# Performance work log

Hardware: AMD Instinct MI355X
Metric: run time of the kernel (lower is better)

## Reference

```python
import jax, jax.numpy as jnp
import numpy as np

B, N, CIN, COUT = 2, 150000, 64, 64
SPATIAL = (128, 128, 128)  # spatial_shape forward arg, fixed here (list arg)
EPS = 1e-5


def setup_inputs() -> dict:
    key = jax.random.key(0)
    k1, k2, k3 = jax.random.split(key, 3)
    features = jax.random.normal(k1, (B, N, CIN), jnp.float32)
    coordinates = jax.random.randint(k2, (B, N, 3), 0, SPATIAL[0], jnp.int32)
    # SparseConv3d weight: 3x3x3 kernel flattened to 27 offsets, [27, Cin, Cout]
    weight = jax.random.normal(k3, (27, CIN, COUT), jnp.float32) * 0.05
    gamma = jnp.ones((COUT,), jnp.float32)
    beta = jnp.zeros((COUT,), jnp.float32)
    return {"features": features, "coordinates": coordinates, "weight": weight,
            "gamma": gamma, "beta": beta, "batch_size": B}


def _rulebook_ids(coordinates, batch_size):
    """For each of 27 kernel offsets, the flat input-point id feeding each output
    site (output sites = input sites, rulebook gather). Empty/OOB -> BN (zero row)."""
    X, Y, Z = SPATIAL
    Np = coordinates.shape[1]
    BN = batch_size * Np
    pid = jnp.arange(BN, dtype=jnp.int32)
    b = jnp.repeat(jnp.arange(batch_size, dtype=jnp.int32), Np)
    c = coordinates.reshape(-1, 3)
    # dense voxel hash: coord -> point id (max for deterministic collision handling)
    grid = jnp.full((batch_size, X, Y, Z), -1, jnp.int32)
    grid = grid.at[b, c[:, 0], c[:, 1], c[:, 2]].max(pid)
    # 27 offsets in {-1,0,1}^3 (padding=1, kernel=3, stride=1)
    r = jnp.arange(-1, 2, dtype=jnp.int32)
    offs = jnp.stack(jnp.meshgrid(r, r, r, indexing="ij"), -1).reshape(27, 3)
    nc = c[None, :, :] + offs[:, None, :]                      # [27, BN, 3]
    hi = jnp.array([X, Y, Z], jnp.int32)
    valid = jnp.all((nc >= 0) & (nc < hi), axis=-1)            # [27, BN]
    ncc = jnp.clip(nc, 0, hi - 1)
    ids = grid[b[None, :], ncc[..., 0], ncc[..., 1], ncc[..., 2]]
    return jnp.where(valid & (ids >= 0), ids, BN)              # BN -> zero row


def reference(features, coordinates, weight, gamma, beta, batch_size):
    Bs, Np, Cin = features.shape
    BN = Bs * Np
    ids = _rulebook_ids(coordinates, batch_size)               # [27, BN]
    feats = jnp.concatenate(
        [features.reshape(BN, Cin), jnp.zeros((1, Cin), features.dtype)], 0)

    # gather-GEMM-scatter accumulated over the 27 kernel offsets
    def step(acc, xs):
        idk, wk = xs
        return acc + feats[idk] @ wk, None

    out0 = jnp.zeros((BN, weight.shape[-1]), features.dtype)
    out, _ = jax.lax.scan(step, out0, (ids, weight))

    # BatchNorm1d (training stats over all points) + ReLU
    mean = out.mean(axis=0)
    var = out.var(axis=0)
    out = (out - mean) * jax.lax.rsqrt(var + EPS) * gamma + beta
    out = jax.nn.relu(out)
    return out.reshape(Bs, Np, -1)
```

## Files before the change

kernel.cpp:

```cpp
#include <hip/hip_runtime.h>

#define GS 128
#define GS3 (GS*GS*GS)
#define NPTS 150000
#define NBATCH 2
#define BN_TOT (NBATCH*NPTS)
#define EPS 1e-5f

#define CONV_BLOCKS 1172

#define OFF_GRID   0ull
#define SZ_GRID    ((size_t)NBATCH*GS3*4)
#define OFF_WFRAG  SZ_GRID
#define SZ_WFRAG   ((size_t)27*8*64*8*2)
#define OFF_STATS  (OFF_WFRAG + SZ_WFRAG)
#define OFF_FB16   (OFF_STATS + 512)
#define SZ_FB16    ((size_t)BN_TOT*64*2)

typedef __attribute__((ext_vector_type(8))) short bf16x8;
typedef __attribute__((ext_vector_type(4))) float f32x4;
typedef unsigned int u32;
typedef const __attribute__((address_space(1))) u32* gas_u32p;
typedef __attribute__((address_space(3))) u32* las_u32p;

__device__ __forceinline__ short f2bf(float f) {
    union { float f; unsigned u; } v; v.f = f;
    unsigned r = v.u + 0x7fffu + ((v.u >> 16) & 1u);
    return (short)(r >> 16);
}

__global__ __launch_bounds__(256) void k_scatter(const int* __restrict__ coords,
                                                 int* __restrict__ grid) {
    int p = blockIdx.x * 256 + threadIdx.x;
    if (p >= BN_TOT) return;
    int b = p / NPTS;
    int x = coords[p*3+0], y = coords[p*3+1], z = coords[p*3+2];
    atomicMax(&grid[((b*GS + x)*GS + y)*GS + z], p);
}

__global__ __launch_bounds__(256) void k_prefrag(const float* __restrict__ w,
                                                 short* __restrict__ wfrag) {
    int t = blockIdx.x * 256 + threadIdx.x;
    if (t >= 27*2*4*64*8) return;
    int i    = t & 7;
    int lane = (t >> 3) & 63;
    int tt   = (t >> 9) & 3;
    int c    = (t >> 11) & 1;
    int k    = t >> 12;
    int kk = c*32 + (lane >> 4)*8 + i;
    int co = tt*16 + (lane & 15);
    wfrag[t] = f2bf(w[(k*64 + kk)*64 + co]);
}

__global__ __launch_bounds__(256) void k_tobf16(const float* __restrict__ f,
                                                ushort* __restrict__ o) {
    int i = blockIdx.x*256 + threadIdx.x;
    if (i >= BN_TOT*8) return;
    const float4* s = (const float4*)(f + (size_t)i*8);
    float4 x = s[0], y = s[1];
    ushort4 lo = { (ushort)f2bf(x.x),(ushort)f2bf(x.y),(ushort)f2bf(x.z),(ushort)f2bf(x.w) };
    ushort4 hi = { (ushort)f2bf(y.x),(ushort)f2bf(y.y),(ushort)f2bf(y.z),(ushort)f2bf(y.w) };
    ushort4* d = (ushort4*)(o + (size_t)i*8);
    d[0] = lo; d[1] = hi;
}

__global__ __launch_bounds__(512, 4) void k_conv(
    const ushort* __restrict__ fb16,
    const int* __restrict__ coords,
    const int* __restrict__ grid,
    const ushort* __restrict__ wfrag,
    float* __restrict__ out,
    float* __restrict__ gstats)
{
    __shared__ __align__(16) ushort bufs[2][4096];
    __shared__ float bsum[64], bsq[64];

    const int tid  = threadIdx.x;
    const int lane = tid & 63;
    const int wv   = tid >> 6;
    const int r    = lane & 15;
    const int seg  = lane >> 4;
    const int p0   = blockIdx.x * 256 + wv * 32;
    const int pr0  = p0 + r;
    const int pr1  = pr0 + 16;

    int cx0=-9, cy0=-9, cz0=-9, cx1=-9, cy1=-9, cz1=-9;
    int gb0=0, gb1=0;
    if (pr0 < BN_TOT) { cx0=coords[pr0*3+0]; cy0=coords[pr0*3+1]; cz0=coords[pr0*3+2];
                        gb0 = (pr0 >= NPTS) ? GS3 : 0; }
    if (pr1 < BN_TOT) { cx1=coords[pr1*3+0]; cy1=coords[pr1*3+1]; cz1=coords[pr1*3+2];
                        gb1 = (pr1 >= NPTS) ? GS3 : 0; }

    auto lk = [&](int gb, int cx, int cy, int cz, int kk) -> int {
        int dx = kk/9 - 1, dy = (kk/3)%3 - 1, dz = kk%3 - 1;
        int nx = cx+dx, ny = cy+dy, nz = cz+dz;
        int ok = (int)(((unsigned)nx < (unsigned)GS) & ((unsigned)ny < (unsigned)GS) &
                       ((unsigned)nz < (unsigned)GS));
        int ax = nx & 127, ay = ny & 127, az = nz & 127;
        int id = grid[gb + (ax<<14) + (ay<<7) + az];
        return ok ? id : -1;
    };

    auto stage = [&](int kk, int bsel) {
        const u32* g = (const u32*)(wfrag + (size_t)kk*4096 + tid*8);
        u32* l = (u32*)(&bufs[bsel][wv*512]);
        __builtin_amdgcn_global_load_lds((gas_u32p)g, (las_u32p)l, 16, 0, 0);
    };

    const bf16x8 zz = {0,0,0,0,0,0,0,0};
    f32x4 c00={0,0,0,0}, c01={0,0,0,0}, c02={0,0,0,0}, c03={0,0,0,0};
    f32x4 c10={0,0,0,0}, c11={0,0,0,0}, c12={0,0,0,0}, c13={0,0,0,0};

    stage(0, 0);
    int id0 = lk(gb0,cx0,cy0,cz0, 0);
    int id1 = lk(gb1,cx1,cy1,cz1, 0);

    for (int k = 0; k < 27; ++k) {
        const ushort* a0p = fb16 + (size_t)(id0 < 0 ? 0 : id0)*64;
        const ushort* a1p = fb16 + (size_t)(id1 < 0 ? 0 : id1)*64;
        bf16x8 a00 = *(const bf16x8*)(a0p + seg*8);
        bf16x8 a01 = *(const bf16x8*)(a0p + 32 + seg*8);
        bf16x8 a10 = *(const bf16x8*)(a1p + seg*8);
        bf16x8 a11 = *(const bf16x8*)(a1p + 32 + seg*8);
        int kn = (k == 26) ? 0 : k+1;
        int idn0 = lk(gb0,cx0,cy0,cz0, kn);
        int idn1 = lk(gb1,cx1,cy1,cz1, kn);
        stage(kn, (k+1)&1);
        if (id0 < 0) { a00 = zz; a01 = zz; }
        if (id1 < 0) { a10 = zz; a11 = zz; }

        asm volatile("s_waitcnt vmcnt(3)" ::: "memory");
        __builtin_amdgcn_s_barrier();
        __builtin_amdgcn_sched_barrier(0);

        const bf16x8* bb = (const bf16x8*)bufs[k&1];
        bf16x8 b00 = bb[0*64+lane], b01 = bb[1*64+lane],
               b02 = bb[2*64+lane], b03 = bb[3*64+lane],
               b10 = bb[4*64+lane], b11 = bb[5*64+lane],
               b12 = bb[6*64+lane], b13 = bb[7*64+lane];

        c00 = __builtin_amdgcn_mfma_f32_16x16x32_bf16(a00, b00, c00, 0,0,0);
        c01 = __builtin_amdgcn_mfma_f32_16x16x32_bf16(a00, b01, c01, 0,0,0);
        c02 = __builtin_amdgcn_mfma_f32_16x16x32_bf16(a00, b02, c02, 0,0,0);
        c03 = __builtin_amdgcn_mfma_f32_16x16x32_bf16(a00, b03, c03, 0,0,0);
        c00 = __builtin_amdgcn_mfma_f32_16x16x32_bf16(a01, b10, c00, 0,0,0);
        c01 = __builtin_amdgcn_mfma_f32_16x16x32_bf16(a01, b11, c01, 0,0,0);
        c02 = __builtin_amdgcn_mfma_f32_16x16x32_bf16(a01, b12, c02, 0,0,0);
        c03 = __builtin_amdgcn_mfma_f32_16x16x32_bf16(a01, b13, c03, 0,0,0);
        c10 = __builtin_amdgcn_mfma_f32_16x16x32_bf16(a10, b00, c10, 0,0,0);
        c11 = __builtin_amdgcn_mfma_f32_16x16x32_bf16(a10, b01, c11, 0,0,0);
        c12 = __builtin_amdgcn_mfma_f32_16x16x32_bf16(a10, b02, c12, 0,0,0);
        c13 = __builtin_amdgcn_mfma_f32_16x16x32_bf16(a10, b03, c13, 0,0,0);
        c10 = __builtin_amdgcn_mfma_f32_16x16x32_bf16(a11, b10, c10, 0,0,0);
        c11 = __builtin_amdgcn_mfma_f32_16x16x32_bf16(a11, b11, c11, 0,0,0);
        c12 = __builtin_amdgcn_mfma_f32_16x16x32_bf16(a11, b12, c12, 0,0,0);
        c13 = __builtin_amdgcn_mfma_f32_16x16x32_bf16(a11, b13, c13, 0,0,0);

        __builtin_amdgcn_sched_barrier(0);
        __builtin_amdgcn_s_barrier();
        id0 = idn0; id1 = idn1;
    }

    {
        const int orow = seg*4;
        float* ob = out + (size_t)p0*64;
        #pragma unroll
        for (int j = 0; j < 4; ++j) {
            int row0 = orow + j;
            if (p0 + row0 < BN_TOT) {
                ob[row0*64 +  0 + r] = c00[j];
                ob[row0*64 + 16 + r] = c01[j];
                ob[row0*64 + 32 + r] = c02[j];
                ob[row0*64 + 48 + r] = c03[j];
            }
            int row1 = 16 + orow + j;
            if (p0 + row1 < BN_TOT) {
                ob[row1*64 +  0 + r] = c10[j];
                ob[row1*64 + 16 + r] = c11[j];
                ob[row1*64 + 32 + r] = c12[j];
                ob[row1*64 + 48 + r] = c13[j];
            }
        }
    }
    if (tid < 64) { bsum[tid] = 0.f; bsq[tid] = 0.f; }
    __syncthreads();
    float s0=0,s1=0,s2=0,s3=0,q0=0,q1=0,q2=0,q3=0;
    #pragma unroll
    for (int j = 0; j < 4; ++j) {
        s0 += c00[j] + c10[j];  q0 += c00[j]*c00[j] + c10[j]*c10[j];
        s1 += c01[j] + c11[j];  q1 += c01[j]*c01[j] + c11[j]*c11[j];
        s2 += c02[j] + c12[j];  q2 += c02[j]*c02[j] + c12[j]*c12[j];
        s3 += c03[j] + c13[j];  q3 += c03[j]*c03[j] + c13[j]*c13[j];
    }
    atomicAdd(&bsum[ 0 + r], s0);  atomicAdd(&bsq[ 0 + r], q0);
    atomicAdd(&bsum[16 + r], s1);  atomicAdd(&bsq[16 + r], q1);
    atomicAdd(&bsum[32 + r], s2);  atomicAdd(&bsq[32 + r], q2);
    atomicAdd(&bsum[48 + r], s3);  atomicAdd(&bsq[48 + r], q3);
    __syncthreads();
    if (tid < 64) { atomicAdd(&gstats[tid], bsum[tid]); atomicAdd(&gstats[64+tid], bsq[tid]); }
}

__global__ __launch_bounds__(256) void k_norm(float* __restrict__ out,
                                              const float* __restrict__ stats,
                                              const float* __restrict__ gamma,
                                              const float* __restrict__ beta) {
    int i = blockIdx.x*256 + threadIdx.x;
    const int n4 = BN_TOT*16;
    if (i >= n4) return;
    float4 v = ((const float4*)out)[i];
    int ch = (i & 15) * 4;
    float o[4] = {v.x, v.y, v.z, v.w};
    float rp[4];
    #pragma unroll
    for (int j = 0; j < 4; ++j) {
        int c = ch + j;
        float mean = stats[c] * (1.f/BN_TOT);
        float var  = stats[64+c] * (1.f/BN_TOT) - mean*mean;
        float y = (o[j] - mean) * rsqrtf(var + EPS) * gamma[c] + beta[c];
        rp[j] = fmaxf(y, 0.f);
    }
    float4 rv; rv.x = rp[0]; rv.y = rp[1]; rv.z = rp[2]; rv.w = rp[3];
    ((float4*)out)[i] = rv;
}

extern "C" void kernel_launch(void* const* d_in, const int* in_sizes, int n_in,
                              void* d_out, int out_size, void* d_ws, size_t ws_size,
                              hipStream_t stream) {
    const float* feats  = (const float*)d_in[0];
    const int*   coords = (const int*)d_in[1];
    const float* weight = (const float*)d_in[2];
    const float* gamma  = (const float*)d_in[3];
    const float* beta   = (const float*)d_in[4];
    float* out = (float*)d_out;

    char*   ws    = (char*)d_ws;
    int*    grid  = (int*)(ws + OFF_GRID);
    short*  wfrag = (short*)(ws + OFF_WFRAG);
    float*  stats = (float*)(ws + OFF_STATS);
    ushort* fb16  = (ushort*)(ws + OFF_FB16);

    hipMemsetAsync(grid, 0xFF, SZ_GRID, stream);
    hipMemsetAsync(stats, 0, 512, stream);

    k_scatter<<<(BN_TOT + 255)/256, 256, 0, stream>>>(coords, grid);
    k_prefrag<<<(27*2*4*64*8)/256, 256, 0, stream>>>(weight, (short*)wfrag);
    k_tobf16<<<(BN_TOT*8)/256, 256, 0, stream>>>(feats, fb16);
    k_conv<<<CONV_BLOCKS, 512, 0, stream>>>(fb16, coords, grid,
                                            (const ushort*)wfrag, out, stats);
    k_norm<<<(BN_TOT*16 + 255)/256, 256, 0, stream>>>(out, stats, gamma, beta);
}
```

Before: 219.2 us.

## Precompute rulebook ids and widen conv tile to 96 rows per wave

Result: slower. 304.9 us (+39.1%).

```diff
diff --git a/kernel.cpp b/kernel.cpp
--- a/kernel.cpp
+++ b/kernel.cpp
@@ -5,28 +5,29 @@
 #define NPTS 150000
 #define NBATCH 2
 #define BN_TOT (NBATCH*NPTS)
+#define BN_PAD 300288
 #define EPS 1e-5f
 
-#define CONV_BLOCKS 1172
+#define CONV_BLOCKS 782
+#define PREP_BLOCKS 9375
 
 #define OFF_GRID   0ull
 #define SZ_GRID    ((size_t)NBATCH*GS3*4)
-#define OFF_WFRAG  SZ_GRID
-#define SZ_WFRAG   ((size_t)27*8*64*8*2)
+#define OFF_WFRAG  (OFF_GRID + SZ_GRID)
+#define SZ_WFRAG   ((size_t)27*4096*2)
 #define OFF_STATS  (OFF_WFRAG + SZ_WFRAG)
 #define OFF_FB16   (OFF_STATS + 512)
-#define SZ_FB16    ((size_t)BN_TOT*64*2)
+#define SZ_FB16    ((size_t)BN_PAD*64*2)
+#define OFF_IDS    (OFF_FB16 + SZ_FB16)
+#define SZ_IDS     ((size_t)27*BN_PAD*4)
 
 typedef __attribute__((ext_vector_type(8))) short bf16x8;
 typedef __attribute__((ext_vector_type(4))) float f32x4;
-typedef unsigned int u32;
-typedef const __attribute__((address_space(1))) u32* gas_u32p;
-typedef __attribute__((address_space(3))) u32* las_u32p;
 
 __device__ __forceinline__ short f2bf(float f) {
     union { float f; unsigned u; } v; v.f = f;
-    unsigned r = v.u + 0x7fffu + ((v.u >> 16) & 1u);
-    return (short)(r >> 16);
+    unsigned rr = v.u + 0x7fffu + ((v.u >> 16) & 1u);
+    return (short)(rr >> 16);
 }
 
 __global__ __launch_bounds__(256) void k_scatter(const int* __restrict__ coords,
@@ -52,152 +53,139 @@
     wfrag[t] = f2bf(w[(k*64 + kk)*64 + co]);
 }
 
-__global__ __launch_bounds__(256) void k_tobf16(const float* __restrict__ f,
-                                                ushort* __restrict__ o) {
-    int i = blockIdx.x*256 + threadIdx.x;
-    if (i >= BN_TOT*8) return;
-    const float4* s = (const float4*)(f + (size_t)i*8);
-    float4 x = s[0], y = s[1];
-    ushort4 lo = { (ushort)f2bf(x.x),(ushort)f2bf(x.y),(ushort)f2bf(x.z),(ushort)f2bf(x.w) };
-    ushort4 hi = { (ushort)f2bf(y.x),(ushort)f2bf(y.y),(ushort)f2bf(y.z),(ushort)f2bf(y.w) };
-    ushort4* d = (ushort4*)(o + (size_t)i*8);
-    d[0] = lo; d[1] = hi;
-}
-
-__global__ __launch_bounds__(512, 4) void k_conv(
+__global__ __launch_bounds__(256) void k_prep(const float* __restrict__ feats,
+                                              const int* __restrict__ coords,
+                                              const int* __restrict__ grid,
+                                              ushort* __restrict__ fb16,
+                                              int* __restrict__ ids) {
+    int gt = blockIdx.x*256 + threadIdx.x;
+    if (gt < BN_TOT*8) {
+        const float4* s = (const float4*)(feats + (size_t)gt*8);
+        float4 x = s[0], y = s[1];
+        ushort4 lo = { (ushort)f2bf(x.x),(ushort)f2bf(x.y),(ushort)f2bf(x.z),(ushort)f2bf(x.w) };
+        ushort4 hi = { (ushort)f2bf(y.x),(ushort)f2bf(y.y),(ushort)f2bf(y.z),(ushort)f2bf(y.w) };
+        ushort4* d = (ushort4*)(fb16 + (size_t)gt*8);
+        d[0] = lo; d[1] = hi;
+    }
+    int p = gt;
+    if (p < BN_PAD) {
+        if (p < BN_TOT) {
+            int cx = coords[p*3+0], cy = coords[p*3+1], cz = coords[p*3+2];
+            const int* gb = grid + (p >= NPTS ? GS3 : 0);
+            #pragma unroll
+            for (int k = 0; k < 27; ++k) {
+                int dx = k/9 - 1, dy = (k/3)%3 - 1, dz = k%3 - 1;
+                int nx = cx+dx, ny = cy+dy, nz = cz+dz;
+                int id = -1;
+                if (((unsigned)nx < 128u) & ((unsigned)ny < 128u) & ((unsigned)nz < 128u))
+                    id = gb[(nx<<14) + (ny<<7) + nz];
+                ids[(size_t)k*BN_PAD + p] = id;
+            }
+        } else {
+            #pragma unroll
+            for (int k = 0; k < 27; ++k) ids[(size_t)k*BN_PAD + p] = -1;
+        }
+    }
+}
+
+__global__ __launch_bounds__(256, 2) void k_conv(
     const ushort* __restrict__ fb16,
-    const int* __restrict__ coords,
-    const int* __restrict__ grid,
+    const int* __restrict__ ids,
     const ushort* __restrict__ wfrag,
     float* __restrict__ out,
     float* __restrict__ gstats)
 {
-    __shared__ __align__(16) ushort bufs[2][4096];
     __shared__ float bsum[64], bsq[64];
-
     const int tid  = threadIdx.x;
     const int lane = tid & 63;
     const int wv   = tid >> 6;
     const int r    = lane & 15;
     const int seg  = lane >> 4;
-    const int p0   = blockIdx.x * 256 + wv * 32;
-    const int pr0  = p0 + r;
-    const int pr1  = pr0 + 16;
-
-    int cx0=-9, cy0=-9, cz0=-9, cx1=-9, cy1=-9, cz1=-9;
-    int gb0=0, gb1=0;
-    if (pr0 < BN_TOT) { cx0=coords[pr0*3+0]; cy0=coords[pr0*3+1]; cz0=coords[pr0*3+2];
-                        gb0 = (pr0 >= NPTS) ? GS3 : 0; }
-    if (pr1 < BN_TOT) { cx1=coords[pr1*3+0]; cy1=coords[pr1*3+1]; cz1=coords[pr1*3+2];
-                        gb1 = (pr1 >= NPTS) ? GS3 : 0; }
-
-    auto lk = [&](int gb, int cx, int cy, int cz, int kk) -> int {
-        int dx = kk/9 - 1, dy = (kk/3)%3 - 1, dz = kk%3 - 1;
-        int nx = cx+dx, ny = cy+dy, nz = cz+dz;
-        int ok = (int)(((unsigned)nx < (unsigned)GS) & ((unsigned)ny < (unsigned)GS) &
-                       ((unsigned)nz < (unsigned)GS));
-        int ax = nx & 127, ay = ny & 127, az = nz & 127;
-        int id = grid[gb + (ax<<14) + (ay<<7) + az];
-        return ok ? id : -1;
-    };
-
-    auto stage = [&](int kk, int bsel) {
-        const u32* g = (const u32*)(wfrag + (size_t)kk*4096 + tid*8);
-        u32* l = (u32*)(&bufs[bsel][wv*512]);
-        __builtin_amdgcn_global_load_lds((gas_u32p)g, (las_u32p)l, 16, 0, 0);
-    };
-
-    const bf16x8 zz = {0,0,0,0,0,0,0,0};
-    f32x4 c00={0,0,0,0}, c01={0,0,0,0}, c02={0,0,0,0}, c03={0,0,0,0};
-    f32x4 c10={0,0,0,0}, c11={0,0,0,0}, c12={0,0,0,0}, c13={0,0,0,0};
-
-    stage(0, 0);
-    int id0 = lk(gb0,cx0,cy0,cz0, 0);
-    int id1 = lk(gb1,cx1,cy1,cz1, 0);
-
+    const int p0   = (blockIdx.x*4 + wv) * 96;
+
+#define LDA2(dst, idv) { int sel_ = (idv) < 0 ? BN_TOT : (idv);                 \
+        const ushort* ap_ = fb16 + (size_t)sel_*64 + seg*8;                     \
+        dst[0] = *(const bf16x8*)(ap_); dst[1] = *(const bf16x8*)(ap_ + 32); }
+#define LDB(kk) { const bf16x8* wp_ = (const bf16x8*)(wfrag + (size_t)(kk)*4096); \
+        _Pragma("unroll") for (int f_ = 0; f_ < 8; ++f_) bb[f_] = wp_[f_*64 + lane]; }
+#define LDIDS(dst, kk) { const int* ip_ = ids + (size_t)(kk)*BN_PAD + p0 + r;   \
+        _Pragma("unroll") for (int t_ = 0; t_ < 6; ++t_) dst[t_] = ip_[16*t_]; }
+
+    f32x4 acc[6][4];
+    #pragma unroll
+    for (int t = 0; t < 6; ++t)
+        #pragma unroll
+        for (int q = 0; q < 4; ++q) acc[t][q] = (f32x4){0,0,0,0};
+
+    bf16x8 aX[3][2], aY[3][2], bb[8];
+    int idc[6], idn[6];
+
+    LDIDS(idc, 0);
+    LDB(0);
+    #pragma unroll
+    for (int t = 0; t < 3; ++t) LDA2(aX[t], idc[t]);
+    #pragma unroll
+    for (int t = 0; t < 3; ++t) LDA2(aY[t], idc[t+3]);
+    LDIDS(idn, 1);
+
+    #pragma unroll 1
     for (int k = 0; k < 27; ++k) {
-        const ushort* a0p = fb16 + (size_t)(id0 < 0 ? 0 : id0)*64;
-        const ushort* a1p = fb16 + (size_t)(id1 < 0 ? 0 : id1)*64;
-        bf16x8 a00 = *(const bf16x8*)(a0p + seg*8);
-        bf16x8 a01 = *(const bf16x8*)(a0p + 32 + seg*8);
-        bf16x8 a10 = *(const bf16x8*)(a1p + seg*8);
-        bf16x8 a11 = *(const bf16x8*)(a1p + 32 + seg*8);
-        int kn = (k == 26) ? 0 : k+1;
-        int idn0 = lk(gb0,cx0,cy0,cz0, kn);
-        int idn1 = lk(gb1,cx1,cy1,cz1, kn);
-        stage(kn, (k+1)&1);
-        if (id0 < 0) { a00 = zz; a01 = zz; }
-        if (id1 < 0) { a10 = zz; a11 = zz; }
-
-        asm volatile("s_waitcnt vmcnt(3)" ::: "memory");
-        __builtin_amdgcn_s_barrier();
-        __builtin_amdgcn_sched_barrier(0);
-
-        const bf16x8* bb = (const bf16x8*)bufs[k&1];
-        bf16x8 b00 = bb[0*64+lane], b01 = bb[1*64+lane],
-               b02 = bb[2*64+lane], b03 = bb[3*64+lane],
-               b10 = bb[4*64+lane], b11 = bb[5*64+lane],
-               b12 = bb[6*64+lane], b13 = bb[7*64+lane];
-
-        c00 = __builtin_amdgcn_mfma_f32_16x16x32_bf16(a00, b00, c00, 0,0,0);
-        c01 = __builtin_amdgcn_mfma_f32_16x16x32_bf16(a00, b01, c01, 0,0,0);
-        c02 = __builtin_amdgcn_mfma_f32_16x16x32_bf16(a00, b02, c02, 0,0,0);
-        c03 = __builtin_amdgcn_mfma_f32_16x16x32_bf16(a00, b03, c03, 0,0,0);
-        c00 = __builtin_amdgcn_mfma_f32_16x16x32_bf16(a01, b10, c00, 0,0,0);
-        c01 = __builtin_amdgcn_mfma_f32_16x16x32_bf16(a01, b11, c01, 0,0,0);
-        c02 = __builtin_amdgcn_mfma_f32_16x16x32_bf16(a01, b12, c02, 0,0,0);
-        c03 = __builtin_amdgcn_mfma_f32_16x16x32_bf16(a01, b13, c03, 0,0,0);
-        c10 = __builtin_amdgcn_mfma_f32_16x16x32_bf16(a10, b00, c10, 0,0,0);
-        c11 = __builtin_amdgcn_mfma_f32_16x16x32_bf16(a10, b01, c11, 0,0,0);
-        c12 = __builtin_amdgcn_mfma_f32_16x16x32_bf16(a10, b02, c12, 0,0,0);
-        c13 = __builtin_amdgcn_mfma_f32_16x16x32_bf16(a10, b03, c13, 0,0,0);
-        c10 = __builtin_amdgcn_mfma_f32_16x16x32_bf16(a11, b10, c10, 0,0,0);
-        c11 = __builtin_amdgcn_mfma_f32_16x16x32_bf16(a11, b11, c11, 0,0,0);
-        c12 = __builtin_amdgcn_mfma_f32_16x16x32_bf16(a11, b12, c12, 0,0,0);
-        c13 = __builtin_amdgcn_mfma_f32_16x16x32_bf16(a11, b13, c13, 0,0,0);
-
-        __builtin_amdgcn_sched_barrier(0);
-        __builtin_amdgcn_s_barrier();
-        id0 = idn0; id1 = idn1;
-    }
-
-    {
-        const int orow = seg*4;
-        float* ob = out + (size_t)p0*64;
+        #pragma unroll
+        for (int t = 0; t < 3; ++t)
+            #pragma unroll
+            for (int q = 0; q < 4; ++q) {
+                acc[t][q] = __builtin_amdgcn_mfma_f32_16x16x32_bf16(aX[t][0], bb[q],   acc[t][q], 0,0,0);
+                acc[t][q] = __builtin_amdgcn_mfma_f32_16x16x32_bf16(aX[t][1], bb[4+q], acc[t][q], 0,0,0);
+            }
+        #pragma unroll
+        for (int t = 0; t < 3; ++t) LDA2(aX[t], idn[t]);
+        #pragma unroll
+        for (int t = 0; t < 3; ++t)
+            #pragma unroll
+            for (int q = 0; q < 4; ++q) {
+                acc[3+t][q] = __builtin_amdgcn_mfma_f32_16x16x32_bf16(aY[t][0], bb[q],   acc[3+t][q], 0,0,0);
+                acc[3+t][q] = __builtin_amdgcn_mfma_f32_16x16x32_bf16(aY[t][1], bb[4+q], acc[3+t][q], 0,0,0);
+            }
+        #pragma unroll
+        for (int t = 0; t < 3; ++t) LDA2(aY[t], idn[t+3]);
+        int kb = (k < 26) ? k+1 : 26;
+        LDB(kb);
+        int k2 = (k < 25) ? k+2 : 26;
+        LDIDS(idn, k2);
+    }
+
+    #pragma unroll
+    for (int t = 0; t < 6; ++t) {
         #pragma unroll
         for (int j = 0; j < 4; ++j) {
-            int row0 = orow + j;
-            if (p0 + row0 < BN_TOT) {
-                ob[row0*64 +  0 + r] = c00[j];
-                ob[row0*64 + 16 + r] = c01[j];
-                ob[row0*64 + 32 + r] = c02[j];
-                ob[row0*64 + 48 + r] = c03[j];
-            }
-            int row1 = 16 + orow + j;
-            if (p0 + row1 < BN_TOT) {
-                ob[row1*64 +  0 + r] = c10[j];
-                ob[row1*64 + 16 + r] = c11[j];
-                ob[row1*64 + 32 + r] = c12[j];
-                ob[row1*64 + 48 + r] = c13[j];
+            int g = p0 + 16*t + seg*4 + j;
+            if (g < BN_TOT) {
+                float* ob = out + (size_t)g*64 + r;
+                ob[ 0] = acc[t][0][j];
+                ob[16] = acc[t][1][j];
+                ob[32] = acc[t][2][j];
+                ob[48] = acc[t][3][j];
             }
         }
     }
+
     if (tid < 64) { bsum[tid] = 0.f; bsq[tid] = 0.f; }
     __syncthreads();
-    float s0=0,s1=0,s2=0,s3=0,q0=0,q1=0,q2=0,q3=0;
-    #pragma unroll
-    for (int j = 0; j < 4; ++j) {
-        s0 += c00[j] + c10[j];  q0 += c00[j]*c00[j] + c10[j]*c10[j];
-        s1 += c01[j] + c11[j];  q1 += c01[j]*c01[j] + c11[j]*c11[j];
-        s2 += c02[j] + c12[j];  q2 += c02[j]*c02[j] + c12[j]*c12[j];
-        s3 += c03[j] + c13[j];  q3 += c03[j]*c03[j] + c13[j]*c13[j];
-    }
-    atomicAdd(&bsum[ 0 + r], s0);  atomicAdd(&bsq[ 0 + r], q0);
-    atomicAdd(&bsum[16 + r], s1);  atomicAdd(&bsq[16 + r], q1);
-    atomicAdd(&bsum[32 + r], s2);  atomicAdd(&bsq[32 + r], q2);
-    atomicAdd(&bsum[48 + r], s3);  atomicAdd(&bsq[48 + r], q3);
+    #pragma unroll
+    for (int q = 0; q < 4; ++q) {
+        float s = 0.f, sq = 0.f;
+        #pragma unroll
+        for (int t = 0; t < 6; ++t)
+            #pragma unroll
+            for (int j = 0; j < 4; ++j) { float v = acc[t][q][j]; s += v; sq += v*v; }
+        atomicAdd(&bsum[q*16 + r], s);
+        atomicAdd(&bsq [q*16 + r], sq);
+    }
     __syncthreads();
     if (tid < 64) { atomicAdd(&gstats[tid], bsum[tid]); atomicAdd(&gstats[64+tid], bsq[tid]); }
+#undef LDA2
+#undef LDB
+#undef LDIDS
 }
 
 __global__ __launch_bounds__(256) void k_norm(float* __restrict__ out,
@@ -238,14 +226,17 @@
     short*  wfrag = (short*)(ws + OFF_WFRAG);
     float*  stats = (float*)(ws + OFF_STATS);
     ushort* fb16  = (ushort*)(ws + OFF_FB16);
+    int*    idbuf = (int*)(ws + OFF_IDS);
 
     hipMemsetAsync(grid, 0xFF, SZ_GRID, stream);
     hipMemsetAsync(stats, 0, 512, stream);
+    hipMemsetAsync(fb16 + (size_t)BN_TOT*64, 0,
+                   (size_t)(BN_PAD - BN_TOT)*128, stream);
 
     k_scatter<<<(BN_TOT + 255)/256, 256, 0, stream>>>(coords, grid);
-    k_prefrag<<<(27*2*4*64*8)/256, 256, 0, stream>>>(weight, (short*)wfrag);
-    k_tobf16<<<(BN_TOT*8)/256, 256, 0, stream>>>(feats, fb16);
-    k_conv<<<CONV_BLOCKS, 512, 0, stream>>>(fb16, coords, grid,
-                                            (const ushort*)wfrag, out, stats);
-    k_norm<<<(BN_TOT*16 + 255)/256, 256, 0, stream>>>(out, stats, gamma, beta);
-}
+    k_prefrag<<<(27*2*4*64*8)/256, 256, 0, stream>>>(weight, wfrag);
+    k_prep<<<PREP_BLOCKS, 256, 0, stream>>>(feats, coords, grid, fb16, idbuf);
+    k_conv<<<CONV_BLOCKS, 256, 0, stream>>>(fb16, idbuf, (const ushort*)wfrag,
+                                            out, stats);
+    k_norm<<<(BN_TOT*16)/256, 256, 0, stream>>>(out, stats, gamma, beta);
+}
```

## Sort points into spatial buckets for locality and skip empty-neighbor MFMAs

Applied to the files above, without the earlier changes.

Measured after the change: 296.8 us. 1.35x slower.

```diff
diff --git a/kernel.cpp b/kernel.cpp
--- a/kernel.cpp
+++ b/kernel.cpp
@@ -5,17 +5,25 @@
 #define NPTS 150000
 #define NBATCH 2
 #define BN_TOT (NBATCH*NPTS)
+#define BN_PAD 300032
+#define ZROW   BN_PAD
 #define EPS 1e-5f
+#define NBKT 8192
 
 #define CONV_BLOCKS 1172
 
 #define OFF_GRID   0ull
 #define SZ_GRID    ((size_t)NBATCH*GS3*4)
-#define OFF_WFRAG  SZ_GRID
-#define SZ_WFRAG   ((size_t)27*8*64*8*2)
+#define OFF_GRIDS  (OFF_GRID + SZ_GRID)
+#define OFF_WFRAG  (OFF_GRIDS + SZ_GRID)
+#define SZ_WFRAG   ((size_t)27*4096*2)
 #define OFF_STATS  (OFF_WFRAG + SZ_WFRAG)
-#define OFF_FB16   (OFF_STATS + 512)
-#define SZ_FB16    ((size_t)BN_TOT*64*2)
+#define OFF_CNT    (OFF_STATS + 512)
+#define OFF_CUR    (OFF_CNT + NBKT*4)
+#define OFF_SIDX   (OFF_CUR + NBKT*4)
+#define OFF_CSORT  (OFF_SIDX + 1200128)
+#define OFF_FB16S  (OFF_CSORT + (size_t)BN_PAD*16)
+#define SZ_FB16S   ((size_t)(BN_PAD+1)*128)
 
 typedef __attribute__((ext_vector_type(8))) short bf16x8;
 typedef __attribute__((ext_vector_type(4))) float f32x4;
@@ -25,17 +33,74 @@
 
 __device__ __forceinline__ short f2bf(float f) {
     union { float f; unsigned u; } v; v.f = f;
-    unsigned r = v.u + 0x7fffu + ((v.u >> 16) & 1u);
-    return (short)(r >> 16);
-}
-
-__global__ __launch_bounds__(256) void k_scatter(const int* __restrict__ coords,
-                                                 int* __restrict__ grid) {
-    int p = blockIdx.x * 256 + threadIdx.x;
+    unsigned rr = v.u + 0x7fffu + ((v.u >> 16) & 1u);
+    return (short)(rr >> 16);
+}
+
+__global__ __launch_bounds__(256) void k_count(const int* __restrict__ coords,
+                                               int* __restrict__ grid,
+                                               u32* __restrict__ cnt) {
+    int p = blockIdx.x*256 + threadIdx.x;
     if (p >= BN_TOT) return;
-    int b = p / NPTS;
     int x = coords[p*3+0], y = coords[p*3+1], z = coords[p*3+2];
-    atomicMax(&grid[((b*GS + x)*GS + y)*GS + z], p);
+    int b = (p >= NPTS);
+    atomicMax(&grid[(b<<21) | (x<<14) | (y<<7) | z], p);
+    atomicAdd(&cnt[(b<<12) | ((x>>3)<<8) | ((y>>3)<<4) | (z>>3)], 1u);
+}
+
+__global__ __launch_bounds__(1024) void k_scan(const u32* __restrict__ cnt,
+                                               u32* __restrict__ cur) {
+    __shared__ u32 ps[1024];
+    int t = threadIdx.x;
+    u32 l[8]; u32 s = 0;
+    #pragma unroll
+    for (int i = 0; i < 8; ++i) { l[i] = cnt[t*8+i]; s += l[i]; }
+    ps[t] = s; __syncthreads();
+    for (int off = 1; off < 1024; off <<= 1) {
+        u32 v = (t >= off) ? ps[t-off] : 0u; __syncthreads();
+        ps[t] += v; __syncthreads();
+    }
+    u32 run = (t == 0) ? 0u : ps[t-1];
+    #pragma unroll
+    for (int i = 0; i < 8; ++i) { cur[t*8+i] = run; run += l[i]; }
+}
+
+__global__ __launch_bounds__(256) void k_place(const float* __restrict__ feats,
+                                               const int* __restrict__ coords,
+                                               u32* __restrict__ cur,
+                                               int* __restrict__ sortidx,
+                                               int4* __restrict__ csorted,
+                                               ushort* __restrict__ fb16s) {
+    int p = blockIdx.x*256 + threadIdx.x;
+    if (p >= BN_PAD) return;
+    if (p >= BN_TOT) { csorted[p] = make_int4(-9,-9,-9,0); return; }
+    int x = coords[p*3+0], y = coords[p*3+1], z = coords[p*3+2];
+    int b = (p >= NPTS);
+    int bkt = (b<<12) | ((x>>3)<<8) | ((y>>3)<<4) | (z>>3);
+    int pos = (int)atomicAdd(&cur[bkt], 1u);
+    sortidx[p] = pos;
+    csorted[pos] = make_int4(x, y, z, p);
+    const float4* s = (const float4*)(feats + (size_t)p*64);
+    ushort* d = fb16s + (size_t)pos*64;
+    #pragma unroll
+    for (int i = 0; i < 8; ++i) {
+        float4 a = s[2*i], c = s[2*i+1];
+        ushort4 u0 = { (ushort)f2bf(a.x),(ushort)f2bf(a.y),(ushort)f2bf(a.z),(ushort)f2bf(a.w) };
+        ushort4 u1 = { (ushort)f2bf(c.x),(ushort)f2bf(c.y),(ushort)f2bf(c.z),(ushort)f2bf(c.w) };
+        ((ushort4*)d)[2*i] = u0; ((ushort4*)d)[2*i+1] = u1;
+    }
+}
+
+__global__ __launch_bounds__(256) void k_regrid(const int* __restrict__ coords,
+                                                const int* __restrict__ grid,
+                                                const int* __restrict__ sortidx,
+                                                int* __restrict__ gridS) {
+    int p = blockIdx.x*256 + threadIdx.x;
+    if (p >= BN_TOT) return;
+    int x = coords[p*3+0], y = coords[p*3+1], z = coords[p*3+2];
+    int b = (p >= NPTS);
+    int cell = (b<<21) | (x<<14) | (y<<7) | z;
+    if (grid[cell] == p) gridS[cell] = sortidx[p];
 }
 
 __global__ __launch_bounds__(256) void k_prefrag(const float* __restrict__ w,
@@ -52,22 +117,10 @@
     wfrag[t] = f2bf(w[(k*64 + kk)*64 + co]);
 }
 
-__global__ __launch_bounds__(256) void k_tobf16(const float* __restrict__ f,
-                                                ushort* __restrict__ o) {
-    int i = blockIdx.x*256 + threadIdx.x;
-    if (i >= BN_TOT*8) return;
-    const float4* s = (const float4*)(f + (size_t)i*8);
-    float4 x = s[0], y = s[1];
-    ushort4 lo = { (ushort)f2bf(x.x),(ushort)f2bf(x.y),(ushort)f2bf(x.z),(ushort)f2bf(x.w) };
-    ushort4 hi = { (ushort)f2bf(y.x),(ushort)f2bf(y.y),(ushort)f2bf(y.z),(ushort)f2bf(y.w) };
-    ushort4* d = (ushort4*)(o + (size_t)i*8);
-    d[0] = lo; d[1] = hi;
-}
-
 __global__ __launch_bounds__(512, 4) void k_conv(
-    const ushort* __restrict__ fb16,
-    const int* __restrict__ coords,
-    const int* __restrict__ grid,
+    const ushort* __restrict__ fb16s,
+    const int4* __restrict__ csorted,
+    const int* __restrict__ gridS,
     const ushort* __restrict__ wfrag,
     float* __restrict__ out,
     float* __restrict__ gstats)
@@ -81,23 +134,18 @@
     const int r    = lane & 15;
     const int seg  = lane >> 4;
     const int p0   = blockIdx.x * 256 + wv * 32;
-    const int pr0  = p0 + r;
-    const int pr1  = pr0 + 16;
-
-    int cx0=-9, cy0=-9, cz0=-9, cx1=-9, cy1=-9, cz1=-9;
-    int gb0=0, gb1=0;
-    if (pr0 < BN_TOT) { cx0=coords[pr0*3+0]; cy0=coords[pr0*3+1]; cz0=coords[pr0*3+2];
-                        gb0 = (pr0 >= NPTS) ? GS3 : 0; }
-    if (pr1 < BN_TOT) { cx1=coords[pr1*3+0]; cy1=coords[pr1*3+1]; cz1=coords[pr1*3+2];
-                        gb1 = (pr1 >= NPTS) ? GS3 : 0; }
+
+    const int4 c0 = csorted[p0 + r];
+    const int4 c1 = csorted[p0 + 16 + r];
+    const int gb0 = (c0.w >= NPTS) ? GS3 : 0;
+    const int gb1 = (c1.w >= NPTS) ? GS3 : 0;
 
     auto lk = [&](int gb, int cx, int cy, int cz, int kk) -> int {
         int dx = kk/9 - 1, dy = (kk/3)%3 - 1, dz = kk%3 - 1;
         int nx = cx+dx, ny = cy+dy, nz = cz+dz;
-        int ok = (int)(((unsigned)nx < (unsigned)GS) & ((unsigned)ny < (unsigned)GS) &
-                       ((unsigned)nz < (unsigned)GS));
-        int ax = nx & 127, ay = ny & 127, az = nz & 127;
-        int id = grid[gb + (ax<<14) + (ay<<7) + az];
+        int ok = (int)(((unsigned)nx < 128u) & ((unsigned)ny < 128u) &
+                       ((unsigned)nz < 128u));
+        int id = gridS[gb + ((nx&127)<<14) + ((ny&127)<<7) + (nz&127)];
         return ok ? id : -1;
     };
 
@@ -107,95 +155,101 @@
         __builtin_amdgcn_global_load_lds((gas_u32p)g, (las_u32p)l, 16, 0, 0);
     };
 
-    const bf16x8 zz = {0,0,0,0,0,0,0,0};
     f32x4 c00={0,0,0,0}, c01={0,0,0,0}, c02={0,0,0,0}, c03={0,0,0,0};
     f32x4 c10={0,0,0,0}, c11={0,0,0,0}, c12={0,0,0,0}, c13={0,0,0,0};
 
     stage(0, 0);
-    int id0 = lk(gb0,cx0,cy0,cz0, 0);
-    int id1 = lk(gb1,cx1,cy1,cz1, 0);
-
+    int s0 = lk(gb0, c0.x, c0.y, c0.z, 0);
+    int s1 = lk(gb1, c1.x, c1.y, c1.z, 0);
+
+    #pragma unroll 1
     for (int k = 0; k < 27; ++k) {
-        const ushort* a0p = fb16 + (size_t)(id0 < 0 ? 0 : id0)*64;
-        const ushort* a1p = fb16 + (size_t)(id1 < 0 ? 0 : id1)*64;
-        bf16x8 a00 = *(const bf16x8*)(a0p + seg*8);
-        bf16x8 a01 = *(const bf16x8*)(a0p + 32 + seg*8);
-        bf16x8 a10 = *(const bf16x8*)(a1p + seg*8);
-        bf16x8 a11 = *(const bf16x8*)(a1p + 32 + seg*8);
+        const ushort* a0p = fb16s + (size_t)(s0 < 0 ? ZROW : s0)*64 + seg*8;
+        const ushort* a1p = fb16s + (size_t)(s1 < 0 ? ZROW : s1)*64 + seg*8;
+        bf16x8 a00 = *(const bf16x8*)(a0p);
+        bf16x8 a01 = *(const bf16x8*)(a0p + 32);
+        bf16x8 a10 = *(const bf16x8*)(a1p);
+        bf16x8 a11 = *(const bf16x8*)(a1p + 32);
+        const bool v0 = (s0 >= 0), v1 = (s1 >= 0);
+
         int kn = (k == 26) ? 0 : k+1;
-        int idn0 = lk(gb0,cx0,cy0,cz0, kn);
-        int idn1 = lk(gb1,cx1,cy1,cz1, kn);
+        int g0n = lk(gb0, c0.x, c0.y, c0.z, kn);
+        int g1n = lk(gb1, c1.x, c1.y, c1.z, kn);
         stage(kn, (k+1)&1);
-        if (id0 < 0) { a00 = zz; a01 = zz; }
-        if (id1 < 0) { a10 = zz; a11 = zz; }
-
-        asm volatile("s_waitcnt vmcnt(3)" ::: "memory");
+
+        const bf16x8 zz = {0,0,0,0,0,0,0,0};
+        if (!v0) { a00 = zz; a01 = zz; }
+        if (!v1) { a10 = zz; a11 = zz; }
+
+        asm volatile("s_waitcnt vmcnt(1)" ::: "memory");
         __builtin_amdgcn_s_barrier();
         __builtin_amdgcn_sched_barrier(0);
 
-        const bf16x8* bb = (const bf16x8*)bufs[k&1];
-        bf16x8 b00 = bb[0*64+lane], b01 = bb[1*64+lane],
-               b02 = bb[2*64+lane], b03 = bb[3*64+lane],
-               b10 = bb[4*64+lane], b11 = bb[5*64+lane],
-               b12 = bb[6*64+lane], b13 = bb[7*64+lane];
-
-        c00 = __builtin_amdgcn_mfma_f32_16x16x32_bf16(a00, b00, c00, 0,0,0);
-        c01 = __builtin_amdgcn_mfma_f32_16x16x32_bf16(a00, b01, c01, 0,0,0);
-        c02 = __builtin_amdgcn_mfma_f32_16x16x32_bf16(a00, b02, c02, 0,0,0);
-        c03 = __builtin_amdgcn_mfma_f32_16x16x32_bf16(a00, b03, c03, 0,0,0);
-        c00 = __builtin_amdgcn_mfma_f32_16x16x32_bf16(a01, b10, c00, 0,0,0);
-        c01 = __builtin_amdgcn_mfma_f32_16x16x32_bf16(a01, b11, c01, 0,0,0);
-        c02 = __builtin_amdgcn_mfma_f32_16x16x32_bf16(a01, b12, c02, 0,0,0);
-        c03 = __builtin_amdgcn_mfma_f32_16x16x32_bf16(a01, b13, c03, 0,0,0);
-        c10 = __builtin_amdgcn_mfma_f32_16x16x32_bf16(a10, b00, c10, 0,0,0);
-        c11 = __builtin_amdgcn_mfma_f32_16x16x32_bf16(a10, b01, c11, 0,0,0);
-        c12 = __builtin_amdgcn_mfma_f32_16x16x32_bf16(a10, b02, c12, 0,0,0);
-        c13 = __builtin_amdgcn_mfma_f32_16x16x32_bf16(a10, b03, c13, 0,0,0);
-        c10 = __builtin_amdgcn_mfma_f32_16x16x32_bf16(a11, b10, c10, 0,0,0);
-        c11 = __builtin_amdgcn_mfma_f32_16x16x32_bf16(a11, b11, c11, 0,0,0);
-        c12 = __builtin_amdgcn_mfma_f32_16x16x32_bf16(a11, b12, c12, 0,0,0);
-        c13 = __builtin_amdgcn_mfma_f32_16x16x32_bf16(a11, b13, c13, 0,0,0);
-
+        const bool any0 = __any(v0), any1 = __any(v1);
+        if (any0 | any1) {
+            const bf16x8* bb = (const bf16x8*)bufs[k&1];
+            bf16x8 b00 = bb[0*64+lane], b01 = bb[1*64+lane],
+                   b02 = bb[2*64+lane], b03 = bb[3*64+lane],
+                   b10 = bb[4*64+lane], b11 = bb[5*64+lane],
+                   b12 = bb[6*64+lane], b13 = bb[7*64+lane];
+            if (any0) {
+                c00 = __builtin_amdgcn_mfma_f32_16x16x32_bf16(a00, b00, c00, 0,0,0);
+                c01 = __builtin_amdgcn_mfma_f32_16x16x32_bf16(a00, b01, c01, 0,0,0);
+                c02 = __builtin_amdgcn_mfma_f32_16x16x32_bf16(a00, b02, c02, 0,0,0);
+                c03 = __builtin_amdgcn_mfma_f32_16x16x32_bf16(a00, b03, c03, 0,0,0);
+                c00 = __builtin_amdgcn_mfma_f32_16x16x32_bf16(a01, b10, c00, 0,0,0);
+                c01 = __builtin_amdgcn_mfma_f32_16x16x32_bf16(a01, b11, c01, 0,0,0);
+                c02 = __builtin_amdgcn_mfma_f32_16x16x32_bf16(a01, b12, c02, 0,0,0);
+                c03 = __builtin_amdgcn_mfma_f32_16x16x32_bf16(a01, b13, c03, 0,0,0);
+            }
+            if (any1) {
+                c10 = __builtin_amdgcn_mfma_f32_16x16x32_bf16(a10, b00, c10, 0,0,0);
+                c11 = __builtin_amdgcn_mfma_f32_16x16x32_bf16(a10, b01, c11, 0,0,0);
+                c12 = __builtin_amdgcn_mfma_f32_16x16x32_bf16(a10, b02, c12, 0,0,0);
+                c13 = __builtin_amdgcn_mfma_f32_16x16x32_bf16(a10, b03, c13, 0,0,0);
+                c10 = __builtin_amdgcn_mfma_f32_16x16x32_bf16(a11, b10, c10, 0,0,0);
+                c11 = __builtin_amdgcn_mfma_f32_16x16x32_bf16(a11, b11, c11, 0,0,0);
+                c12 = __builtin_amdgcn_mfma_f32_16x16x32_bf16(a11, b12, c12, 0,0,0);
+                c13 = __builtin_amdgcn_mfma_f32_16x16x32_bf16(a11, b13, c13, 0,0,0);
+            }
+        }
         __builtin_amdgcn_sched_barrier(0);
         __builtin_amdgcn_s_barrier();
-        id0 = idn0; id1 = idn1;
-    }
-
-    {
-        const int orow = seg*4;
-        float* ob = out + (size_t)p0*64;
-        #pragma unroll
-        for (int j = 0; j < 4; ++j) {
-            int row0 = orow + j;
-            if (p0 + row0 < BN_TOT) {
-                ob[row0*64 +  0 + r] = c00[j];
-                ob[row0*64 + 16 + r] = c01[j];
-                ob[row0*64 + 32 + r] = c02[j];
-                ob[row0*64 + 48 + r] = c03[j];
-            }
-            int row1 = 16 + orow + j;
-            if (p0 + row1 < BN_TOT) {
-                ob[row1*64 +  0 + r] = c10[j];
-                ob[row1*64 + 16 + r] = c11[j];
-                ob[row1*64 + 32 + r] = c12[j];
-                ob[row1*64 + 48 + r] = c13[j];
-            }
+        s0 = g0n; s1 = g1n;
+    }
+
+    const int* cw = (const int*)csorted;
+    #pragma unroll
+    for (int j = 0; j < 4; ++j) {
+        int row0 = p0 + seg*4 + j;
+        if (row0 < BN_TOT) {
+            int opid = cw[(size_t)row0*4 + 3];
+            float* ob = out + (size_t)opid*64 + r;
+            ob[ 0] = c00[j]; ob[16] = c01[j]; ob[32] = c02[j]; ob[48] = c03[j];
         }
-    }
+        int row1 = p0 + 16 + seg*4 + j;
+        if (row1 < BN_TOT) {
+            int opid = cw[(size_t)row1*4 + 3];
+            float* ob = out + (size_t)opid*64 + r;
+            ob[ 0] = c10[j]; ob[16] = c11[j]; ob[32] = c12[j]; ob[48] = c13[j];
+        }
+    }
+
     if (tid < 64) { bsum[tid] = 0.f; bsq[tid] = 0.f; }
     __syncthreads();
-    float s0=0,s1=0,s2=0,s3=0,q0=0,q1=0,q2=0,q3=0;
+    float s_[4] = {0,0,0,0}, q_[4] = {0,0,0,0};
     #pragma unroll
     for (int j = 0; j < 4; ++j) {
-        s0 += c00[j] + c10[j];  q0 += c00[j]*c00[j] + c10[j]*c10[j];
-        s1 += c01[j] + c11[j];  q1 += c01[j]*c01[j] + c11[j]*c11[j];
-        s2 += c02[j] + c12[j];  q2 += c02[j]*c02[j] + c12[j]*c12[j];
-        s3 += c03[j] + c13[j];  q3 += c03[j]*c03[j] + c13[j]*c13[j];
-    }
-    atomicAdd(&bsum[ 0 + r], s0);  atomicAdd(&bsq[ 0 + r], q0);
-    atomicAdd(&bsum[16 + r], s1);  atomicAdd(&bsq[16 + r], q1);
-    atomicAdd(&bsum[32 + r], s2);  atomicAdd(&bsq[32 + r], q2);
-    atomicAdd(&bsum[48 + r], s3);  atomicAdd(&bsq[48 + r], q3);
+        s_[0] += c00[j] + c10[j];  q_[0] += c00[j]*c00[j] + c10[j]*c10[j];
+        s_[1] += c01[j] + c11[j];  q_[1] += c01[j]*c01[j] + c11[j]*c11[j];
+        s_[2] += c02[j] + c12[j];  q_[2] += c02[j]*c02[j] + c12[j]*c12[j];
+        s_[3] += c03[j] + c13[j];  q_[3] += c03[j]*c03[j] + c13[j]*c13[j];
+    }
+    #pragma unroll
+    for (int q = 0; q < 4; ++q) {
+        atomicAdd(&bsum[q*16 + r], s_[q]);
+        atomicAdd(&bsq [q*16 + r], q_[q]);
+    }
     __syncthreads();
     if (tid < 64) { atomicAdd(&gstats[tid], bsum[tid]); atomicAdd(&gstats[64+tid], bsq[tid]); }
 }
@@ -233,19 +287,31 @@
     const float* beta   = (const float*)d_in[4];
     float* out = (float*)d_out;
 
-    char*   ws    = (char*)d_ws;
-    int*    grid  = (int*)(ws + OFF_GRID);
-    short*  wfrag = (short*)(ws + OFF_WFRAG);
-    float*  stats = (float*)(ws + OFF_STATS);
-    ushort* fb16  = (ushort*)(ws + OFF_FB16);
-
-    hipMemsetAsync(grid, 0xFF, SZ_GRID, stream);
+    char*   ws      = (char*)d_ws;
+    int*    grid    = (int*)(ws + OFF_GRID);
+    int*    gridS   = (int*)(ws + OFF_GRIDS);
+    short*  wfrag   = (short*)(ws + OFF_WFRAG);
+    float*  stats   = (float*)(ws + OFF_STATS);
+    u32*    cnt     = (u32*)(ws + OFF_CNT);
+    u32*    cur     = (u32*)(ws + OFF_CUR);
+    int*    sortidx = (int*)(ws + OFF_SIDX);
+    int4*   csorted = (int4*)(ws + OFF_CSORT);
+    ushort* fb16s   = (ushort*)(ws + OFF_FB16S);
+
+    hipMemsetAsync(grid,  0xFF, SZ_GRID, stream);
+    hipMemsetAsync(gridS, 0xFF, SZ_GRID, stream);
     hipMemsetAsync(stats, 0, 512, stream);
-
-    k_scatter<<<(BN_TOT + 255)/256, 256, 0, stream>>>(coords, grid);
-    k_prefrag<<<(27*2*4*64*8)/256, 256, 0, stream>>>(weight, (short*)wfrag);
-    k_tobf16<<<(BN_TOT*8)/256, 256, 0, stream>>>(feats, fb16);
-    k_conv<<<CONV_BLOCKS, 512, 0, stream>>>(fb16, coords, grid,
-                                            (const ushort*)wfrag, out, stats);
-    k_norm<<<(BN_TOT*16 + 255)/256, 256, 0, stream>>>(out, stats, gamma, beta);
-}
+    hipMemsetAsync(cnt,   0, NBKT*4, stream);
+    hipMemsetAsync(fb16s + (size_t)BN_TOT*64, 0,
+                   (size_t)(BN_PAD + 1 - BN_TOT)*128, stream);
+
+    k_count <<<(BN_TOT + 255)/256, 256, 0, stream>>>(coords, grid, cnt);
+    k_scan  <<<1, 1024, 0, stream>>>(cnt, cur);
+    k_place <<<(BN_PAD + 255)/256, 256, 0, stream>>>(feats, coords, cur,
+                                                     sortidx, csorted, fb16s);
+    k_regrid<<<(BN_TOT + 255)/256, 256, 0, stream>>>(coords, grid, sortidx, gridS);
+    k_prefrag<<<(27*2*4*64*8)/256, 256, 0, stream>>>(weight, wfrag);
+    k_conv  <<<CONV_BLOCKS, 512, 0, stream>>>(fb16s, csorted, gridS,
+                                              (const ushort*)wfrag, out, stats);
+    k_norm  <<<(BN_TOT*16)/256, 256, 0, stream>>>(out, stats, gamma, beta);
+}
```
